# Optimization experiments

Hardware: AMD Instinct MI355X
Metric: run time of the kernel (lower is better)

The kernel has to match this reference:

```python
import jax, jax.numpy as jnp
import numpy as np

N, H, L, O = 8192, 512, 3, 512
LN_EPS = 1e-5


def setup_inputs() -> dict:
    key = jax.random.key(0)
    ks = jax.random.split(key, 8)
    # sparse symmetric adjacency with positive weights, zero diagonal
    u = jax.random.uniform(ks[0], (N, N))
    w = jax.random.uniform(ks[1], (N, N)) * 0.9 + 0.1
    A = jnp.where(u < 0.004, w, 0.0)
    A = (A + A.T) * 0.5
    A = A * (1.0 - jnp.eye(N, dtype=A.dtype))
    s = 0.02
    return {
        "node_feat": jax.random.normal(ks[2], (1, N, H), jnp.float32),
        "adj": A[None],
        "conv_w": jax.random.normal(ks[3], (L, H, H), jnp.float32) * s,
        "conv_b": jnp.zeros((L, H), jnp.float32),
        "mlp_w": jax.random.normal(ks[4], (L, H, H), jnp.float32) * s,
        "mlp_b": jnp.zeros((L, H), jnp.float32),
        "ln_g": jnp.ones((L, H), jnp.float32),
        "ln_b": jnp.zeros((L, H), jnp.float32),
        "lin_w": jax.random.normal(ks[5], (H, O), jnp.float32) * s,
        "lin_b": jnp.zeros((O,), jnp.float32),
    }


def _layer_norm(x, g, b):
    mu = jnp.mean(x, axis=-1, keepdims=True)
    var = jnp.mean(jnp.square(x - mu), axis=-1, keepdims=True)
    return (x - mu) * jax.lax.rsqrt(var + LN_EPS) * g + b


def reference(node_feat, adj, conv_w, conv_b, mlp_w, mlp_b, ln_g, ln_b, lin_w, lin_b):
    x = node_feat[0]          # [N, H]
    A = adj[0]                # [N, N]
    A = jnp.where(A > 0, A, 0.0)  # edges are positive entries only
    # gcn_norm: add self-loops (weight 1) only where missing
    d = jnp.diagonal(A)
    A1 = A + jnp.diag(jnp.where(d > 0, 0.0, 1.0))
    # deg scattered at target (edge_index[1] = column)
    deg = jnp.sum(A1, axis=0)
    dinv = jnp.where(deg > 0, deg ** -0.5, 0.0)
    Ahat = dinv[:, None] * A1 * dinv[None, :]  # [N, N]
    for l in range(L):
        # GCNConv: linear, propagate (aggregate at col), bias
        x = Ahat.T @ (x @ conv_w[l]) + conv_b[l]
        # MLP: Linear -> LayerNorm -> ReLU
        x = jax.nn.relu(_layer_norm(x @ mlp_w[l] + mlp_b[l], ln_g[l], ln_b[l]))
    mu = (x @ lin_w + lin_b)[None]  # [1, N, O]
    return mu
```

## Files before the change

### kernel.cpp

```cpp
#include <hip/hip_runtime.h>

#define NN 8192
#define HD 512
#define NL 3
#define CAP 128
#define LN_EPS 1e-5f

typedef _Float16 f16;
typedef _Float16 f16x8 __attribute__((ext_vector_type(8)));
typedef _Float16 f16x4 __attribute__((ext_vector_type(4)));
typedef float f32x4 __attribute__((ext_vector_type(4)));

__device__ __forceinline__ unsigned short f16_bits(f16 h) {
  union { f16 h; unsigned short u; } x; x.h = h; return x.u;
}
__device__ __forceinline__ f16 bits_f16(unsigned short u) {
  union { unsigned short u; f16 h; } x; x.u = u; return x.h;
}

__global__ __launch_bounds__(256) void k_prep(const float* __restrict__ A,
                                              unsigned* __restrict__ ell,
                                              int* __restrict__ nnz4,
                                              float* __restrict__ dinv) {
  __shared__ float rowbuf[NN];
  __shared__ int wtot[4];
  __shared__ float wsum[4];
  const int r = blockIdx.x;
  const int t = threadIdx.x;
  const int lane = t & 63;
  const int wv = t >> 6;
  const float4* ar = (const float4*)(A + (size_t)r * NN);
  unsigned* er = ell + (size_t)r * CAP;

  int c = 0;
  float s = 0.f;
  for (int i = t; i < NN / 4; i += 256) {
    float4 v = ar[i];
    ((float4*)rowbuf)[i] = v;
    c += (v.x > 0.f) + (v.y > 0.f) + (v.z > 0.f) + (v.w > 0.f);
    s += v.x + v.y + v.z + v.w;
  }
  int inc = c;
  #pragma unroll
  for (int d = 1; d < 64; d <<= 1) {
    int v = __shfl_up(inc, d);
    if (lane >= d) inc += v;
  }
  float ss = s;
  #pragma unroll
  for (int m = 1; m < 64; m <<= 1) ss += __shfl_xor(ss, m);
  if (lane == 63) wtot[wv] = inc;
  if (lane == 0) wsum[wv] = ss;
  __syncthreads();
  int base = inc - c;
  for (int w = 0; w < wv; w++) base += wtot[w];

  int o = base;
  for (int i = t; i < NN / 4; i += 256) {
    float4 v = ((float4*)rowbuf)[i];
    float vals[4] = {v.x, v.y, v.z, v.w};
    #pragma unroll
    for (int q = 0; q < 4; q++) {
      float val = vals[q];
      if (val > 0.f) {
        if (o < CAP) er[o] = ((unsigned)f16_bits((f16)val) << 16) | (unsigned)(i * 4 + q);
        o++;
      }
    }
  }
  if (t == 255) {
    int ne = wtot[0] + wtot[1] + wtot[2] + wtot[3];
    if (ne < CAP) er[ne] = (0x3C00u << 16) | (unsigned)r;
    int ne1 = ne + 1; if (ne1 > CAP) ne1 = CAP;
    int n4 = (ne1 + 3) & ~3;
    for (int k = ne1; k < n4; k++) er[k] = (unsigned)r;
    nnz4[r] = n4;
    float deg = wsum[0] + wsum[1] + wsum[2] + wsum[3] + 1.f;
    dinv[r] = rsqrtf(deg);
  }
}

__global__ __launch_bounds__(256) void k_scalex(const float* __restrict__ x0,
                                                const float* __restrict__ dinv,
                                                f16* __restrict__ xs) {
  const size_t idx = (size_t)blockIdx.x * 256 + threadIdx.x;
  const float4 v = ((const float4*)x0)[idx];
  const float s = dinv[(int)(idx >> 7)];
  f16x4 o = {(f16)(v.x * s), (f16)(v.y * s), (f16)(v.z * s), (f16)(v.w * s)};
  ((f16x4*)xs)[idx] = o;
}

__global__ __launch_bounds__(256) void k_spmm(const unsigned* __restrict__ ell,
                                              const int* __restrict__ nnz4,
                                              const float* __restrict__ dinv,
                                              const f16* __restrict__ xs,
                                              f16* __restrict__ y) {
  const int r = blockIdx.x * 4 + (threadIdx.x >> 6);
  const int lane = threadIdx.x & 63;
  const unsigned* er = ell + (size_t)r * CAP;
  const int ne = nnz4[r];
  float acc[8] = {0.f, 0.f, 0.f, 0.f, 0.f, 0.f, 0.f, 0.f};
  for (int e = 0; e < ne; e += 4) {
    const unsigned w0 = er[e], w1 = er[e + 1], w2 = er[e + 2], w3 = er[e + 3];
    const f16x8 x0 = *(const f16x8*)(xs + (size_t)(w0 & 0xFFFFu) * HD + lane * 8);
    const f16x8 x1 = *(const f16x8*)(xs + (size_t)(w1 & 0xFFFFu) * HD + lane * 8);
    const f16x8 x2 = *(const f16x8*)(xs + (size_t)(w2 & 0xFFFFu) * HD + lane * 8);
    const f16x8 x3 = *(const f16x8*)(xs + (size_t)(w3 & 0xFFFFu) * HD + lane * 8);
    const float f0 = (float)bits_f16((unsigned short)(w0 >> 16));
    const float f1 = (float)bits_f16((unsigned short)(w1 >> 16));
    const float f2 = (float)bits_f16((unsigned short)(w2 >> 16));
    const float f3 = (float)bits_f16((unsigned short)(w3 >> 16));
    #pragma unroll
    for (int j = 0; j < 8; j++) {
      float a = acc[j];
      a = fmaf(f0, (float)x0[j], a);
      a = fmaf(f1, (float)x1[j], a);
      a = fmaf(f2, (float)x2[j], a);
      a = fmaf(f3, (float)x3[j], a);
      acc[j] = a;
    }
  }
  const float s = dinv[r];
  f16x8 o;
  #pragma unroll
  for (int j = 0; j < 8; j++) o[j] = (f16)(acc[j] * s);
  *(f16x8*)(y + (size_t)r * HD + lane * 8) = o;
}

__global__ __launch_bounds__(256) void k_gemm_direct(const f16* __restrict__ A,
                                                     const f16* __restrict__ BT,
                                                     float* __restrict__ C,
                                                     const float* __restrict__ bias) {
  const int t = threadIdx.x;
  const int lane = t & 63;
  const int wave = t >> 6;
  const int wm = wave >> 1, wn = wave & 1;
  const int m0 = blockIdx.x * 128, n0 = blockIdx.y * 128;
  const int rl = lane & 15, kg = (lane >> 4) * 8;

  const f16* aP[4];
  const f16* bP[4];
  #pragma unroll
  for (int i = 0; i < 4; i++)
    aP[i] = A + (size_t)(m0 + wm * 64 + i * 16 + rl) * HD + kg;
  #pragma unroll
  for (int j = 0; j < 4; j++)
    bP[j] = BT + (size_t)(n0 + wn * 64 + j * 16 + rl) * HD + kg;

  f32x4 acc[4][4];
  #pragma unroll
  for (int i = 0; i < 4; i++)
    #pragma unroll
    for (int j = 0; j < 4; j++) {
      f32x4 z = {0.f, 0.f, 0.f, 0.f};
      acc[i][j] = z;
    }

  #pragma unroll 4
  for (int ks = 0; ks < HD; ks += 32) {
    f16x8 af[4], bf[4];
    #pragma unroll
    for (int i = 0; i < 4; i++) af[i] = *(const f16x8*)(aP[i] + ks);
    #pragma unroll
    for (int j = 0; j < 4; j++) bf[j] = *(const f16x8*)(bP[j] + ks);
    #pragma unroll
    for (int i = 0; i < 4; i++)
      #pragma unroll
      for (int j = 0; j < 4; j++)
        acc[i][j] = __builtin_amdgcn_mfma_f32_16x16x32_f16(af[i], bf[j], acc[i][j], 0, 0, 0);
  }

  const int cg = lane >> 4, cl = lane & 15;
  #pragma unroll
  for (int i = 0; i < 4; i++) {
    #pragma unroll
    for (int j = 0; j < 4; j++) {
      const int col = n0 + wn * 64 + j * 16 + cl;
      const float bv = bias ? bias[col] : 0.f;
      #pragma unroll
      for (int rr = 0; rr < 4; rr++) {
        const int row = m0 + wm * 64 + i * 16 + cg * 4 + rr;
        C[(size_t)row * HD + col] = acc[i][j][rr] + bv;
      }
    }
  }
}

__global__ __launch_bounds__(256) void k_wcomb(const float* __restrict__ convw,
                                               const float* __restrict__ mlpw,
                                               f16* __restrict__ WlT) {
  const int l = blockIdx.y;
  const int m0 = blockIdx.x * 8;
  const float* Wc = convw + (size_t)l * HD * HD;
  const float* Wm = mlpw + (size_t)l * HD * HD;
  f16* o = WlT + (size_t)l * HD * HD;
  const int n = threadIdx.x;
  float a0[8] = {0, 0, 0, 0, 0, 0, 0, 0};
  float a1[8] = {0, 0, 0, 0, 0, 0, 0, 0};
  for (int k = 0; k < HD; k++) {
    const float w0 = Wm[(size_t)k * HD + n];
    const float w1 = Wm[(size_t)k * HD + n + 256];
    #pragma unroll
    for (int mi = 0; mi < 8; mi++) {
      const float wc = Wc[(size_t)(m0 + mi) * HD + k];
      a0[mi] = fmaf(wc, w0, a0[mi]);
      a1[mi] = fmaf(wc, w1, a1[mi]);
    }
  }
  #pragma unroll
  for (int mi = 0; mi < 8; mi++) {
    o[(size_t)n * HD + m0 + mi] = (f16)a0[mi];
    o[(size_t)(n + 256) * HD + m0 + mi] = (f16)a1[mi];
  }
}

__global__ void k_bcomb(const float* __restrict__ convb, const float* __restrict__ mlpw,
                        const float* __restrict__ mlpb, float* __restrict__ bl) {
  const int l = blockIdx.x;
  const int n = threadIdx.x;
  const float* Wm = mlpw + (size_t)l * HD * HD;
  float acc = mlpb[l * HD + n];
  for (int k = 0; k < HD; k++) acc = fmaf(convb[l * HD + k], Wm[(size_t)k * HD + n], acc);
  bl[l * HD + n] = acc;
}

__global__ __launch_bounds__(256) void k_twl(const float* __restrict__ lw,
                                             f16* __restrict__ lwT) {
  const int k = blockIdx.x;
  for (int n = threadIdx.x; n < HD; n += 256)
    lwT[(size_t)n * HD + k] = (f16)lw[(size_t)k * HD + n];
}

__global__ __launch_bounds__(256) void k_ln(const float* __restrict__ Hb,
                                            const float* __restrict__ g,
                                            const float* __restrict__ b,
                                            const float* __restrict__ dscale,
                                            f16* __restrict__ outp) {
  const int row = blockIdx.x * 4 + (threadIdx.x >> 6);
  const int lane = threadIdx.x & 63;
  const float4* hr = (const float4*)(Hb + (size_t)row * HD);
  float4 v0 = hr[lane * 2], v1 = hr[lane * 2 + 1];
  float vals[8] = {v0.x, v0.y, v0.z, v0.w, v1.x, v1.y, v1.z, v1.w};
  float s = 0.f, sq = 0.f;
  #pragma unroll
  for (int q = 0; q < 8; q++) { s += vals[q]; sq += vals[q] * vals[q]; }
  #pragma unroll
  for (int m = 1; m < 64; m <<= 1) { s += __shfl_xor(s, m); sq += __shfl_xor(sq, m); }
  const float mu = s * (1.f / HD);
  const float rs = rsqrtf(sq * (1.f / HD) - mu * mu + LN_EPS);
  const float dsc = dscale ? dscale[row] : 1.f;
  f16x8 o;
  #pragma unroll
  for (int q = 0; q < 8; q++) {
    const int c = lane * 8 + q;
    o[q] = (f16)(fmaxf((vals[q] - mu) * rs * g[c] + b[c], 0.f) * dsc);
  }
  *(f16x8*)(outp + (size_t)row * HD + lane * 8) = o;
}

extern "C" void kernel_launch(void* const* d_in, const int* in_sizes, int n_in,
                              void* d_out, int out_size, void* d_ws, size_t ws_size,
                              hipStream_t stream) {
  const float* node_feat = (const float*)d_in[0];
  const float* adj       = (const float*)d_in[1];
  const float* conv_w    = (const float*)d_in[2];
  const float* conv_b    = (const float*)d_in[3];
  const float* mlp_w     = (const float*)d_in[4];
  const float* mlp_b     = (const float*)d_in[5];
  const float* ln_g      = (const float*)d_in[6];
  const float* ln_b      = (const float*)d_in[7];
  const float* lin_w     = (const float*)d_in[8];
  const float* lin_b     = (const float*)d_in[9];
  float* out = (float*)d_out;

  char* p = (char*)d_ws;
  unsigned* ell = (unsigned*)p; p += (size_t)NN * CAP * 4;
  int* nnz4  = (int*)p;   p += (size_t)NN * 4;
  float* dinv = (float*)p; p += (size_t)NN * 4;
  f16* xsA   = (f16*)p;   p += (size_t)NN * HD * 2;
  f16* xsB   = (f16*)p;   p += (size_t)NN * HD * 2;
  f16* ybuf  = (f16*)p;   p += (size_t)NN * HD * 2;
  float* hbuf = (float*)p; p += (size_t)NN * HD * 4;
  f16* WlT   = (f16*)p;   p += (size_t)NL * HD * HD * 2;
  f16* lwT   = (f16*)p;   p += (size_t)HD * HD * 2;
  float* bl  = (float*)p; p += (size_t)NL * HD * 4;

  k_prep<<<NN, 256, 0, stream>>>(adj, ell, nnz4, dinv);
  k_scalex<<<NN * HD / 4 / 256, 256, 0, stream>>>(node_feat, dinv, xsA);
  k_wcomb<<<dim3(64, NL), 256, 0, stream>>>(conv_w, mlp_w, WlT);
  k_bcomb<<<NL, HD, 0, stream>>>(conv_b, mlp_w, mlp_b, bl);
  k_twl<<<HD, 256, 0, stream>>>(lin_w, lwT);

  f16* xcur = xsA;
  for (int l = 0; l < NL; l++) {
    k_spmm<<<NN / 4, 256, 0, stream>>>(ell, nnz4, dinv, xcur, ybuf);
    k_gemm_direct<<<dim3(64, 4), 256, 0, stream>>>(ybuf, WlT + (size_t)l * HD * HD,
                                                   hbuf, bl + l * HD);
    f16* nxt = (xcur == xsA) ? xsB : xsA;
    k_ln<<<NN / 4, 256, 0, stream>>>(hbuf, ln_g + l * HD, ln_b + l * HD,
                                     (l < 2) ? dinv : nullptr, nxt);
    xcur = nxt;
  }
  k_gemm_direct<<<dim3(64, 4), 256, 0, stream>>>(xcur, lwT, out, lin_b);
}
```

Before: 367.7 us.

## Fuse GEMM with LayerNorm, unroll SpMM by 8, keep prep row in registers

Replaces the per-layer GEMM that wrote an fp32 hidden buffer plus a separate LayerNorm kernel with one kernel. Each 512-thread block computes 16 full rows via MFMA and applies bias, LayerNorm, ReLU and scaling in place, using a small shared reduction across waves. This removes the fp32 intermediate round trip and one launch per layer. The SpMM inner loop now gathers 8 neighbours per iteration (ELL padded to multiples of 8) for more memory-level parallelism, and the prep kernel holds the adjacency row in registers instead of shared memory. The risk is that the fused GEMM reads its A and B fragments straight from global memory with no shared-memory tiling, and that the extra padding adds dummy gathers.

```diff
diff --git a/kernel.cpp b/kernel.cpp
--- a/kernel.cpp
+++ b/kernel.cpp
@@ -20,9 +20,8 @@
 
 __global__ __launch_bounds__(256) void k_prep(const float* __restrict__ A,
                                               unsigned* __restrict__ ell,
-                                              int* __restrict__ nnz4,
+                                              int* __restrict__ nnz8,
                                               float* __restrict__ dinv) {
-  __shared__ float rowbuf[NN];
   __shared__ int wtot[4];
   __shared__ float wsum[4];
   const int r = blockIdx.x;
@@ -32,19 +31,20 @@
   const float4* ar = (const float4*)(A + (size_t)r * NN);
   unsigned* er = ell + (size_t)r * CAP;
 
+  float4 v[8];
   int c = 0;
   float s = 0.f;
-  for (int i = t; i < NN / 4; i += 256) {
-    float4 v = ar[i];
-    ((float4*)rowbuf)[i] = v;
-    c += (v.x > 0.f) + (v.y > 0.f) + (v.z > 0.f) + (v.w > 0.f);
-    s += v.x + v.y + v.z + v.w;
+  #pragma unroll
+  for (int i = 0; i < 8; i++) {
+    v[i] = ar[t + i * 256];
+    c += (v[i].x > 0.f) + (v[i].y > 0.f) + (v[i].z > 0.f) + (v[i].w > 0.f);
+    s += v[i].x + v[i].y + v[i].z + v[i].w;
   }
   int inc = c;
   #pragma unroll
   for (int d = 1; d < 64; d <<= 1) {
-    int v = __shfl_up(inc, d);
-    if (lane >= d) inc += v;
+    int vv = __shfl_up(inc, d);
+    if (lane >= d) inc += vv;
   }
   float ss = s;
   #pragma unroll
@@ -56,14 +56,14 @@
   for (int w = 0; w < wv; w++) base += wtot[w];
 
   int o = base;
-  for (int i = t; i < NN / 4; i += 256) {
-    float4 v = ((float4*)rowbuf)[i];
-    float vals[4] = {v.x, v.y, v.z, v.w};
+  #pragma unroll
+  for (int i = 0; i < 8; i++) {
+    float vals[4] = {v[i].x, v[i].y, v[i].z, v[i].w};
     #pragma unroll
     for (int q = 0; q < 4; q++) {
       float val = vals[q];
       if (val > 0.f) {
-        if (o < CAP) er[o] = ((unsigned)f16_bits((f16)val) << 16) | (unsigned)(i * 4 + q);
+        if (o < CAP) er[o] = ((unsigned)f16_bits((f16)val) << 16) | (unsigned)((t + i * 256) * 4 + q);
         o++;
       }
     }
@@ -72,9 +72,9 @@
     int ne = wtot[0] + wtot[1] + wtot[2] + wtot[3];
     if (ne < CAP) er[ne] = (0x3C00u << 16) | (unsigned)r;
     int ne1 = ne + 1; if (ne1 > CAP) ne1 = CAP;
-    int n4 = (ne1 + 3) & ~3;
-    for (int k = ne1; k < n4; k++) er[k] = (unsigned)r;
-    nnz4[r] = n4;
+    int n8 = (ne1 + 7) & ~7;
+    for (int k = ne1; k < n8; k++) er[k] = (unsigned)r;
+    nnz8[r] = n8;
     float deg = wsum[0] + wsum[1] + wsum[2] + wsum[3] + 1.f;
     dinv[r] = rsqrtf(deg);
   }
@@ -91,32 +91,31 @@
 }
 
 __global__ __launch_bounds__(256) void k_spmm(const unsigned* __restrict__ ell,
-                                              const int* __restrict__ nnz4,
+                                              const int* __restrict__ nnz8,
                                               const float* __restrict__ dinv,
                                               const f16* __restrict__ xs,
                                               f16* __restrict__ y) {
-  const int r = blockIdx.x * 4 + (threadIdx.x >> 6);
+  const int r = __builtin_amdgcn_readfirstlane(blockIdx.x * 4 + (threadIdx.x >> 6));
   const int lane = threadIdx.x & 63;
   const unsigned* er = ell + (size_t)r * CAP;
-  const int ne = nnz4[r];
+  const int ne = nnz8[r];
   float acc[8] = {0.f, 0.f, 0.f, 0.f, 0.f, 0.f, 0.f, 0.f};
-  for (int e = 0; e < ne; e += 4) {
-    const unsigned w0 = er[e], w1 = er[e + 1], w2 = er[e + 2], w3 = er[e + 3];
-    const f16x8 x0 = *(const f16x8*)(xs + (size_t)(w0 & 0xFFFFu) * HD + lane * 8);
-    const f16x8 x1 = *(const f16x8*)(xs + (size_t)(w1 & 0xFFFFu) * HD + lane * 8);
-    const f16x8 x2 = *(const f16x8*)(xs + (size_t)(w2 & 0xFFFFu) * HD + lane * 8);
-    const f16x8 x3 = *(const f16x8*)(xs + (size_t)(w3 & 0xFFFFu) * HD + lane * 8);
-    const float f0 = (float)bits_f16((unsigned short)(w0 >> 16));
-    const float f1 = (float)bits_f16((unsigned short)(w1 >> 16));
-    const float f2 = (float)bits_f16((unsigned short)(w2 >> 16));
-    const float f3 = (float)bits_f16((unsigned short)(w3 >> 16));
+  for (int e = 0; e < ne; e += 8) {
+    unsigned wv[8];
+    f16x8 xv[8];
+    float fw[8];
+    #pragma unroll
+    for (int q = 0; q < 8; q++) wv[q] = er[e + q];
+    #pragma unroll
+    for (int q = 0; q < 8; q++)
+      xv[q] = *(const f16x8*)(xs + (size_t)(wv[q] & 0xFFFFu) * HD + lane * 8);
+    #pragma unroll
+    for (int q = 0; q < 8; q++) fw[q] = (float)bits_f16((unsigned short)(wv[q] >> 16));
     #pragma unroll
     for (int j = 0; j < 8; j++) {
       float a = acc[j];
-      a = fmaf(f0, (float)x0[j], a);
-      a = fmaf(f1, (float)x1[j], a);
-      a = fmaf(f2, (float)x2[j], a);
-      a = fmaf(f3, (float)x3[j], a);
+      #pragma unroll
+      for (int q = 0; q < 8; q++) a = fmaf(fw[q], (float)xv[q][j], a);
       acc[j] = a;
     }
   }
@@ -125,6 +124,74 @@
   #pragma unroll
   for (int j = 0; j < 8; j++) o[j] = (f16)(acc[j] * s);
   *(f16x8*)(y + (size_t)r * HD + lane * 8) = o;
+}
+
+__global__ __launch_bounds__(512) void k_gemm_ln(const f16* __restrict__ y,
+                                                 const f16* __restrict__ WT,
+                                                 const float* __restrict__ bias,
+                                                 const float* __restrict__ g,
+                                                 const float* __restrict__ bb,
+                                                 const float* __restrict__ dscale,
+                                                 f16* __restrict__ outp) {
+  __shared__ float red[16][8][2];
+  const int t = threadIdx.x;
+  const int lane = t & 63;
+  const int w = t >> 6;
+  const int m0 = blockIdx.x * 16;
+  const int rl = lane & 15, kg = (lane >> 4) * 8;
+  const int nc0 = w * 64;
+  const f16* aP = y + (size_t)(m0 + rl) * HD + kg;
+  const f16* bP = WT + (size_t)(nc0 + rl) * HD + kg;
+
+  f32x4 acc[4];
+  #pragma unroll
+  for (int j = 0; j < 4; j++) { f32x4 z = {0.f, 0.f, 0.f, 0.f}; acc[j] = z; }
+
+  #pragma unroll 2
+  for (int ks = 0; ks < HD; ks += 32) {
+    const f16x8 af = *(const f16x8*)(aP + ks);
+    #pragma unroll
+    for (int j = 0; j < 4; j++) {
+      const f16x8 bf = *(const f16x8*)(bP + (size_t)j * 16 * HD + ks);
+      acc[j] = __builtin_amdgcn_mfma_f32_16x16x32_f16(af, bf, acc[j], 0, 0, 0);
+    }
+  }
+
+  const int cg = lane >> 4, cl = lane & 15;
+  float av[4][4];
+  #pragma unroll
+  for (int j = 0; j < 4; j++) {
+    const float bv = bias[nc0 + j * 16 + cl];
+    #pragma unroll
+    for (int r = 0; r < 4; r++) av[j][r] = acc[j][r] + bv;
+  }
+  #pragma unroll
+  for (int r = 0; r < 4; r++) {
+    float s = av[0][r] + av[1][r] + av[2][r] + av[3][r];
+    float sq = av[0][r] * av[0][r] + av[1][r] * av[1][r] +
+               av[2][r] * av[2][r] + av[3][r] * av[3][r];
+    #pragma unroll
+    for (int m = 1; m < 16; m <<= 1) { s += __shfl_xor(s, m); sq += __shfl_xor(sq, m); }
+    if (cl == 0) { red[cg * 4 + r][w][0] = s; red[cg * 4 + r][w][1] = sq; }
+  }
+  __syncthreads();
+  #pragma unroll
+  for (int r = 0; r < 4; r++) {
+    const int rb = cg * 4 + r;
+    float s = 0.f, sq = 0.f;
+    #pragma unroll
+    for (int q = 0; q < 8; q++) { s += red[rb][q][0]; sq += red[rb][q][1]; }
+    const float mu = s * (1.f / HD);
+    const float rs = rsqrtf(sq * (1.f / HD) - mu * mu + LN_EPS);
+    const int row = m0 + rb;
+    const float dsc = dscale ? dscale[row] : 1.f;
+    #pragma unroll
+    for (int j = 0; j < 4; j++) {
+      const int col = nc0 + j * 16 + cl;
+      const float val = fmaxf((av[j][r] - mu) * rs * g[col] + bb[col], 0.f) * dsc;
+      outp[(size_t)row * HD + col] = (f16)val;
+    }
+  }
 }
 
 __global__ __launch_bounds__(256) void k_gemm_direct(const f16* __restrict__ A,
@@ -231,33 +298,6 @@
     lwT[(size_t)n * HD + k] = (f16)lw[(size_t)k * HD + n];
 }
 
-__global__ __launch_bounds__(256) void k_ln(const float* __restrict__ Hb,
-                                            const float* __restrict__ g,
-                                            const float* __restrict__ b,
-                                            const float* __restrict__ dscale,
-                                            f16* __restrict__ outp) {
-  const int row = blockIdx.x * 4 + (threadIdx.x >> 6);
-  const int lane = threadIdx.x & 63;
-  const float4* hr = (const float4*)(Hb + (size_t)row * HD);
-  float4 v0 = hr[lane * 2], v1 = hr[lane * 2 + 1];
-  float vals[8] = {v0.x, v0.y, v0.z, v0.w, v1.x, v1.y, v1.z, v1.w};
-  float s = 0.f, sq = 0.f;
-  #pragma unroll
-  for (int q = 0; q < 8; q++) { s += vals[q]; sq += vals[q] * vals[q]; }
-  #pragma unroll
-  for (int m = 1; m < 64; m <<= 1) { s += __shfl_xor(s, m); sq += __shfl_xor(sq, m); }
-  const float mu = s * (1.f / HD);
-  const float rs = rsqrtf(sq * (1.f / HD) - mu * mu + LN_EPS);
-  const float dsc = dscale ? dscale[row] : 1.f;
-  f16x8 o;
-  #pragma unroll
-  for (int q = 0; q < 8; q++) {
-    const int c = lane * 8 + q;
-    o[q] = (f16)(fmaxf((vals[q] - mu) * rs * g[c] + b[c], 0.f) * dsc);
-  }
-  *(f16x8*)(outp + (size_t)row * HD + lane * 8) = o;
-}
-
 extern "C" void kernel_launch(void* const* d_in, const int* in_sizes, int n_in,
                               void* d_out, int out_size, void* d_ws, size_t ws_size,
                               hipStream_t stream) {
@@ -275,17 +315,16 @@
 
   char* p = (char*)d_ws;
   unsigned* ell = (unsigned*)p; p += (size_t)NN * CAP * 4;
-  int* nnz4  = (int*)p;   p += (size_t)NN * 4;
+  int* nnz8  = (int*)p;   p += (size_t)NN * 4;
   float* dinv = (float*)p; p += (size_t)NN * 4;
   f16* xsA   = (f16*)p;   p += (size_t)NN * HD * 2;
   f16* xsB   = (f16*)p;   p += (size_t)NN * HD * 2;
   f16* ybuf  = (f16*)p;   p += (size_t)NN * HD * 2;
-  float* hbuf = (float*)p; p += (size_t)NN * HD * 4;
   f16* WlT   = (f16*)p;   p += (size_t)NL * HD * HD * 2;
   f16* lwT   = (f16*)p;   p += (size_t)HD * HD * 2;
   float* bl  = (float*)p; p += (size_t)NL * HD * 4;
 
-  k_prep<<<NN, 256, 0, stream>>>(adj, ell, nnz4, dinv);
+  k_prep<<<NN, 256, 0, stream>>>(adj, ell, nnz8, dinv);
   k_scalex<<<NN * HD / 4 / 256, 256, 0, stream>>>(node_feat, dinv, xsA);
   k_wcomb<<<dim3(64, NL), 256, 0, stream>>>(conv_w, mlp_w, WlT);
   k_bcomb<<<NL, HD, 0, stream>>>(conv_b, mlp_w, mlp_b, bl);
@@ -293,12 +332,11 @@
 
   f16* xcur = xsA;
   for (int l = 0; l < NL; l++) {
-    k_spmm<<<NN / 4, 256, 0, stream>>>(ell, nnz4, dinv, xcur, ybuf);
-    k_gemm_direct<<<dim3(64, 4), 256, 0, stream>>>(ybuf, WlT + (size_t)l * HD * HD,
-                                                   hbuf, bl + l * HD);
+    k_spmm<<<NN / 4, 256, 0, stream>>>(ell, nnz8, dinv, xcur, ybuf);
     f16* nxt = (xcur == xsA) ? xsB : xsA;
-    k_ln<<<NN / 4, 256, 0, stream>>>(hbuf, ln_g + l * HD, ln_b + l * HD,
-                                     (l < 2) ? dinv : nullptr, nxt);
+    k_gemm_ln<<<NN / 16, 512, 0, stream>>>(ybuf, WlT + (size_t)l * HD * HD,
+                                           bl + l * HD, ln_g + l * HD, ln_b + l * HD,
+                                           (l < 2) ? dinv : nullptr, nxt);
     xcur = nxt;
   }
   k_gemm_direct<<<dim3(64, 4), 256, 0, stream>>>(xcur, lwT, out, lin_b);
```

New measurement: 399.2 us. +8.6%, slower.

## Split SpMM into column chunks, pad ELL to 8, store GEMM output as fp16

Applied to the files above, without the earlier changes.

The SpMM now launches four times as many blocks. Each block handles one 128-column chunk, each lane covers 2 columns instead of 8, and the row index is made wave-uniform with readfirstlane. Edge loads are batched 8 at a time, so ELL rows are padded to multiples of 8. The intent is higher occupancy and more memory-level parallelism in the gather, at the cost of reading the ELL indices four times and issuing narrower 4-byte gathers. Separately, the per-layer GEMM writes an fp16 hidden buffer that LayerNorm reads, halving that intermediate traffic at some precision risk before the normalization.

```diff
diff --git a/kernel.cpp b/kernel.cpp
--- a/kernel.cpp
+++ b/kernel.cpp
@@ -9,6 +9,7 @@
 typedef _Float16 f16;
 typedef _Float16 f16x8 __attribute__((ext_vector_type(8)));
 typedef _Float16 f16x4 __attribute__((ext_vector_type(4)));
+typedef _Float16 f16x2 __attribute__((ext_vector_type(2)));
 typedef float f32x4 __attribute__((ext_vector_type(4)));
 
 __device__ __forceinline__ unsigned short f16_bits(f16 h) {
@@ -20,7 +21,7 @@
 
 __global__ __launch_bounds__(256) void k_prep(const float* __restrict__ A,
                                               unsigned* __restrict__ ell,
-                                              int* __restrict__ nnz4,
+                                              int* __restrict__ nnz8,
                                               float* __restrict__ dinv) {
   __shared__ float rowbuf[NN];
   __shared__ int wtot[4];
@@ -72,9 +73,9 @@
     int ne = wtot[0] + wtot[1] + wtot[2] + wtot[3];
     if (ne < CAP) er[ne] = (0x3C00u << 16) | (unsigned)r;
     int ne1 = ne + 1; if (ne1 > CAP) ne1 = CAP;
-    int n4 = (ne1 + 3) & ~3;
-    for (int k = ne1; k < n4; k++) er[k] = (unsigned)r;
-    nnz4[r] = n4;
+    int n8 = (ne1 + 7) & ~7;
+    for (int k = ne1; k < n8; k++) er[k] = (unsigned)r;
+    nnz8[r] = n8;
     float deg = wsum[0] + wsum[1] + wsum[2] + wsum[3] + 1.f;
     dinv[r] = rsqrtf(deg);
   }
@@ -91,45 +92,43 @@
 }
 
 __global__ __launch_bounds__(256) void k_spmm(const unsigned* __restrict__ ell,
-                                              const int* __restrict__ nnz4,
+                                              const int* __restrict__ nnz8,
                                               const float* __restrict__ dinv,
                                               const f16* __restrict__ xs,
                                               f16* __restrict__ y) {
-  const int r = blockIdx.x * 4 + (threadIdx.x >> 6);
+  const int bid = blockIdx.x;
+  const int chunk = bid >> 11;
+  const int rb = bid & 2047;
+  const int r = __builtin_amdgcn_readfirstlane(rb * 4 + (threadIdx.x >> 6));
   const int lane = threadIdx.x & 63;
+  const int c0 = chunk * 128 + lane * 2;
   const unsigned* er = ell + (size_t)r * CAP;
-  const int ne = nnz4[r];
-  float acc[8] = {0.f, 0.f, 0.f, 0.f, 0.f, 0.f, 0.f, 0.f};
-  for (int e = 0; e < ne; e += 4) {
-    const unsigned w0 = er[e], w1 = er[e + 1], w2 = er[e + 2], w3 = er[e + 3];
-    const f16x8 x0 = *(const f16x8*)(xs + (size_t)(w0 & 0xFFFFu) * HD + lane * 8);
-    const f16x8 x1 = *(const f16x8*)(xs + (size_t)(w1 & 0xFFFFu) * HD + lane * 8);
-    const f16x8 x2 = *(const f16x8*)(xs + (size_t)(w2 & 0xFFFFu) * HD + lane * 8);
-    const f16x8 x3 = *(const f16x8*)(xs + (size_t)(w3 & 0xFFFFu) * HD + lane * 8);
-    const float f0 = (float)bits_f16((unsigned short)(w0 >> 16));
-    const float f1 = (float)bits_f16((unsigned short)(w1 >> 16));
-    const float f2 = (float)bits_f16((unsigned short)(w2 >> 16));
-    const float f3 = (float)bits_f16((unsigned short)(w3 >> 16));
-    #pragma unroll
-    for (int j = 0; j < 8; j++) {
-      float a = acc[j];
-      a = fmaf(f0, (float)x0[j], a);
-      a = fmaf(f1, (float)x1[j], a);
-      a = fmaf(f2, (float)x2[j], a);
-      a = fmaf(f3, (float)x3[j], a);
-      acc[j] = a;
+  const int ne = nnz8[r];
+  float a0 = 0.f, a1 = 0.f;
+  for (int e = 0; e < ne; e += 8) {
+    unsigned wv[8];
+    #pragma unroll
+    for (int q = 0; q < 8; q++) wv[q] = er[e + q];
+    f16x2 xv[8];
+    #pragma unroll
+    for (int q = 0; q < 8; q++)
+      xv[q] = *(const f16x2*)(xs + (size_t)(wv[q] & 0xFFFFu) * HD + c0);
+    #pragma unroll
+    for (int q = 0; q < 8; q++) {
+      const float fw = (float)bits_f16((unsigned short)(wv[q] >> 16));
+      a0 = fmaf(fw, (float)xv[q][0], a0);
+      a1 = fmaf(fw, (float)xv[q][1], a1);
     }
   }
   const float s = dinv[r];
-  f16x8 o;
-  #pragma unroll
-  for (int j = 0; j < 8; j++) o[j] = (f16)(acc[j] * s);
-  *(f16x8*)(y + (size_t)r * HD + lane * 8) = o;
+  f16x2 o = {(f16)(a0 * s), (f16)(a1 * s)};
+  *(f16x2*)(y + (size_t)r * HD + c0) = o;
 }
 
 __global__ __launch_bounds__(256) void k_gemm_direct(const f16* __restrict__ A,
                                                      const f16* __restrict__ BT,
-                                                     float* __restrict__ C,
+                                                     float* __restrict__ Cf,
+                                                     f16* __restrict__ Ch,
                                                      const float* __restrict__ bias) {
   const int t = threadIdx.x;
   const int lane = t & 63;
@@ -180,7 +179,9 @@
       #pragma unroll
       for (int rr = 0; rr < 4; rr++) {
         const int row = m0 + wm * 64 + i * 16 + cg * 4 + rr;
-        C[(size_t)row * HD + col] = acc[i][j][rr] + bv;
+        const float v = acc[i][j][rr] + bv;
+        if (Cf) Cf[(size_t)row * HD + col] = v;
+        else Ch[(size_t)row * HD + col] = (f16)v;
       }
     }
   }
@@ -231,16 +232,17 @@
     lwT[(size_t)n * HD + k] = (f16)lw[(size_t)k * HD + n];
 }
 
-__global__ __launch_bounds__(256) void k_ln(const float* __restrict__ Hb,
+__global__ __launch_bounds__(256) void k_ln(const f16* __restrict__ Hb,
                                             const float* __restrict__ g,
                                             const float* __restrict__ b,
                                             const float* __restrict__ dscale,
                                             f16* __restrict__ outp) {
   const int row = blockIdx.x * 4 + (threadIdx.x >> 6);
   const int lane = threadIdx.x & 63;
-  const float4* hr = (const float4*)(Hb + (size_t)row * HD);
-  float4 v0 = hr[lane * 2], v1 = hr[lane * 2 + 1];
-  float vals[8] = {v0.x, v0.y, v0.z, v0.w, v1.x, v1.y, v1.z, v1.w};
+  const f16x8 hv = *(const f16x8*)(Hb + (size_t)row * HD + lane * 8);
+  float vals[8];
+  #pragma unroll
+  for (int q = 0; q < 8; q++) vals[q] = (float)hv[q];
   float s = 0.f, sq = 0.f;
   #pragma unroll
   for (int q = 0; q < 8; q++) { s += vals[q]; sq += vals[q] * vals[q]; }
@@ -275,17 +277,17 @@
 
   char* p = (char*)d_ws;
   unsigned* ell = (unsigned*)p; p += (size_t)NN * CAP * 4;
-  int* nnz4  = (int*)p;   p += (size_t)NN * 4;
+  int* nnz8  = (int*)p;   p += (size_t)NN * 4;
   float* dinv = (float*)p; p += (size_t)NN * 4;
   f16* xsA   = (f16*)p;   p += (size_t)NN * HD * 2;
   f16* xsB   = (f16*)p;   p += (size_t)NN * HD * 2;
   f16* ybuf  = (f16*)p;   p += (size_t)NN * HD * 2;
-  float* hbuf = (float*)p; p += (size_t)NN * HD * 4;
+  f16* hbuf  = (f16*)p;   p += (size_t)NN * HD * 2;
   f16* WlT   = (f16*)p;   p += (size_t)NL * HD * HD * 2;
   f16* lwT   = (f16*)p;   p += (size_t)HD * HD * 2;
   float* bl  = (float*)p; p += (size_t)NL * HD * 4;
 
-  k_prep<<<NN, 256, 0, stream>>>(adj, ell, nnz4, dinv);
+  k_prep<<<NN, 256, 0, stream>>>(adj, ell, nnz8, dinv);
   k_scalex<<<NN * HD / 4 / 256, 256, 0, stream>>>(node_feat, dinv, xsA);
   k_wcomb<<<dim3(64, NL), 256, 0, stream>>>(conv_w, mlp_w, WlT);
   k_bcomb<<<NL, HD, 0, stream>>>(conv_b, mlp_w, mlp_b, bl);
@@ -293,13 +295,13 @@
 
   f16* xcur = xsA;
   for (int l = 0; l < NL; l++) {
-    k_spmm<<<NN / 4, 256, 0, stream>>>(ell, nnz4, dinv, xcur, ybuf);
+    k_spmm<<<NN * 4 / 4, 256, 0, stream>>>(ell, nnz8, dinv, xcur, ybuf);
     k_gemm_direct<<<dim3(64, 4), 256, 0, stream>>>(ybuf, WlT + (size_t)l * HD * HD,
-                                                   hbuf, bl + l * HD);
+                                                   nullptr, hbuf, bl + l * HD);
     f16* nxt = (xcur == xsA) ? xsB : xsA;
     k_ln<<<NN / 4, 256, 0, stream>>>(hbuf, ln_g + l * HD, ln_b + l * HD,
                                      (l < 2) ? dinv : nullptr, nxt);
     xcur = nxt;
   }
-  k_gemm_direct<<<dim3(64, 4), 256, 0, stream>>>(xcur, lwT, out, lin_b);
-}
+  k_gemm_direct<<<dim3(64, 4), 256, 0, stream>>>(xcur, lwT, out, nullptr, lin_b);
+}
```

New measurement: 367.7 us. No clear change (+0.0%).
